# Kernel tuning notes

Hardware: AMD Instinct MI355X
Metric: run time of the kernel (lower is better)

## Reference

```python
import jax, jax.numpy as jnp
import numpy as np

NUM_EXPERTS = 8
PHM_DIM = 4


def setup_inputs() -> dict:
    key = jax.random.key(0)
    k1, k2, k3, k4 = jax.random.split(key, 4)
    bsz, seq, D, O, E, p = 4, 2048, 2048, 2048, NUM_EXPERTS, PHM_DIM
    hidden_states = jax.random.normal(k1, (bsz, seq, D), dtype=jnp.float32)
    gate_w = jax.random.normal(k2, (D, E), dtype=jnp.float32) * 0.02
    phm_rule = jax.random.normal(k3, (E, p, p, p), dtype=jnp.float32) * 0.1
    W = jax.random.normal(k4, (E, p, D // p, O // p), dtype=jnp.float32) * 0.02
    b = jnp.zeros((E, O), dtype=jnp.float32)
    return {"hidden_states": hidden_states, "gate_w": gate_w,
            "phm_rule": phm_rule, "W": W, "b": b}


def reference(hidden_states, gate_w, phm_rule, W, b):
    bsz, seq, dim = hidden_states.shape
    E = gate_w.shape[1]
    x = hidden_states.reshape(-1, dim)                      # [T, D]
    logits = x @ gate_w                                     # [T, E]
    prob = jax.nn.softmax(logits, axis=-1)                  # [T, E]
    gate = jnp.argmax(prob, axis=-1)                        # [T]
    # load-balancing loss
    num_tokens = jnp.sum(jax.nn.one_hot(gate, E, dtype=jnp.int32), axis=0)  # [E]
    f = num_tokens.astype(prob.dtype)
    f = f / jnp.sum(f)
    P = jnp.mean(prob, axis=0)
    balance_loss = E * jnp.sum(P * f)
    # PHM weight per expert: H_e = sum_p kron(phm_rule[e,p], W[e,p]) -> [E, D, O]
    Wfull = jnp.einsum('epab,epij->eaibj', phm_rule, W).reshape(E, dim, -1)
    # dense evaluation of every expert on every token, then top-1 select
    all_out = jnp.einsum('td,edo->teo', x, Wfull) + b[None, :, :]  # [T, E, O]
    tok_prob = jnp.take_along_axis(prob, gate[:, None], axis=1)    # [T, 1]
    out = jnp.take_along_axis(all_out, gate[:, None, None], axis=1)[:, 0, :] * tok_prob
    out = out.reshape(bsz, seq, -1)
    return out, balance_loss, num_tokens
```

## Files before the change

### kernel.cpp

```cpp
#include <hip/hip_runtime.h>
#include <cstdint>
#include <cstddef>

typedef _Float16 f16;
typedef f16 f16x2 __attribute__((ext_vector_type(2)));
typedef f16 f16x4 __attribute__((ext_vector_type(4)));
typedef f16 f16x8 __attribute__((ext_vector_type(8)));
typedef float f32x4 __attribute__((ext_vector_type(4)));

#define NEXP 8
#define BM 128
#define BN 128
#define BK 32
#define NSTAGE 3

__device__ __forceinline__ void async_cp16(void* lds, const void* gsrc) {
  __builtin_amdgcn_global_load_lds(
      (const __attribute__((address_space(1))) void*)gsrc,
      (__attribute__((address_space(3))) void*)lds, 16, 0, 0);
}

__global__ __launch_bounds__(256) void k_gwT(const float* __restrict__ gw,
                                             float* __restrict__ gwT, int D) {
  int i = blockIdx.x * 256 + threadIdx.x;
  int e = i / D, d = i - e * D;
  gwT[i] = gw[d * NEXP + e];
}

__global__ __launch_bounds__(256) void k_gate(
    const float* __restrict__ x, const float* __restrict__ gwT,
    f16* __restrict__ xb, int* __restrict__ gate, float* __restrict__ scale,
    int* __restrict__ cnt, float* __restrict__ probsum, int D)
{
  __shared__ float ps[NEXP];
  __shared__ int pc[NEXP];
  int tid = threadIdx.x, lane = tid & 63, w = tid >> 6;
  if (tid < NEXP) { ps[tid] = 0.f; pc[tid] = 0; }
  __syncthreads();

  int t = blockIdx.x * 4 + w;
  const float* xr = x + (size_t)t * D;
  f16* xbr = xb + (size_t)t * D;

  float acc[NEXP] = {};
  for (int d0 = lane * 4; d0 < D; d0 += 256) {
    float4 v = *(const float4*)(xr + d0);
    f16x4 h; h[0] = (f16)v.x; h[1] = (f16)v.y; h[2] = (f16)v.z; h[3] = (f16)v.w;
    *(f16x4*)(xbr + d0) = h;
#pragma unroll
    for (int e = 0; e < NEXP; e++) {
      float4 g = *(const float4*)(gwT + (size_t)e * D + d0);
      acc[e] += v.x * g.x + v.y * g.y + v.z * g.z + v.w * g.w;
    }
  }
#pragma unroll
  for (int e = 0; e < NEXP; e++) {
    float v = acc[e];
    for (int o = 32; o > 0; o >>= 1) v += __shfl_xor(v, o);
    acc[e] = v;
  }
  if (lane == 0) {
    float m = acc[0]; int g = 0;
#pragma unroll
    for (int e = 1; e < NEXP; e++) if (acc[e] > m) { m = acc[e]; g = e; }
    float pr[NEXP]; float ssum = 0.f;
#pragma unroll
    for (int e = 0; e < NEXP; e++) { pr[e] = __expf(acc[e] - m); ssum += pr[e]; }
    float inv = 1.0f / ssum;
#pragma unroll
    for (int e = 0; e < NEXP; e++) atomicAdd(&ps[e], pr[e] * inv);
    atomicAdd(&pc[g], 1);
    gate[t] = g;
    scale[t] = pr[g] * inv;
  }
  __syncthreads();
  if (tid < NEXP) {
    atomicAdd(&probsum[tid], ps[tid]);
    atomicAdd(&cnt[tid], pc[tid]);
  }
}

__global__ __launch_bounds__(256) void k_wfull(
    const float* __restrict__ Wp, const float* __restrict__ rule,
    f16* __restrict__ wt, int Dp, int Op, int D, int O)
{
  int bid = blockIdx.x;
  int it = Dp >> 5, jt = Op >> 5;
  int itile = bid % it; bid /= it;
  int jtile = bid % jt; bid /= jt;
  int e = bid;
  int i0 = itile * 32, j0 = jtile * 32;

  __shared__ float Wt[4][32][33];
  int tid = threadIdx.x;
  for (int idx = tid; idx < 4096; idx += 256) {
    int p = idx >> 10, rem = idx & 1023, ii = rem >> 5, jj = rem & 31;
    Wt[p][ii][jj] = Wp[(size_t)((e * 4 + p) * Dp + i0 + ii) * Op + j0 + jj];
  }
  __syncthreads();

  int r = tid >> 1;
  int b = r >> 5;
  int jj = r & 31;
  int h = tid & 1;

  float s[4][4];
#pragma unroll
  for (int p = 0; p < 4; p++)
#pragma unroll
    for (int a = 0; a < 4; a++)
      s[p][a] = rule[((e * 4 + p) * 4 + a) * 4 + b];

  f16x8 outv[4][2];
#pragma unroll
  for (int k = 0; k < 16; k++) {
    int i = h * 16 + k;
    float w0 = Wt[0][i][jj], w1 = Wt[1][i][jj];
    float w2 = Wt[2][i][jj], w3 = Wt[3][i][jj];
#pragma unroll
    for (int a = 0; a < 4; a++) {
      float acc = s[0][a] * w0 + s[1][a] * w1 + s[2][a] * w2 + s[3][a] * w3;
      outv[a][k >> 3][k & 7] = (f16)acc;
    }
  }

  size_t rowbase = ((size_t)e * O + (size_t)b * Op + j0 + jj) * D + i0 + h * 16;
#pragma unroll
  for (int a = 0; a < 4; a++) {
    *(f16x8*)(wt + rowbase + (size_t)a * Dp)     = outv[a][0];
    *(f16x8*)(wt + rowbase + (size_t)a * Dp + 8) = outv[a][1];
  }
}

__global__ __launch_bounds__(128) void k_plan(
    const int* __restrict__ cnt, const float* __restrict__ probsum,
    int* __restrict__ offs, int* __restrict__ ndesc,
    int2* __restrict__ desc, float* __restrict__ otail, int T)
{
  __shared__ int soffs[NEXP + 1];
  __shared__ int snd;
  __shared__ float sloss;
  __shared__ int2 sdesc[96];
  int tid = threadIdx.x;
  if (tid == 0) {
    int off = 0, nd = 0; float loss = 0.f;
    for (int e = 0; e < NEXP; e++) {
      soffs[e] = off;
      int c = cnt[e];
      loss += probsum[e] * (float)c;
      for (int m0 = 0; m0 < c; m0 += BM) { sdesc[nd] = make_int2(e, m0); nd++; }
      off += c;
    }
    soffs[NEXP] = off;
    snd = nd;
    sloss = loss;
  }
  __syncthreads();
  if (tid <= NEXP) offs[tid] = soffs[tid];
  if (tid == 9) *ndesc = snd;
  if (tid == 10) {
    float invT = 1.0f / (float)T;
    otail[0] = (float)NEXP * sloss * invT * invT;
  }
  if (tid >= 16 && tid < 16 + NEXP) otail[1 + tid - 16] = (float)cnt[tid - 16];
  for (int i = tid; i < snd; i += 128) desc[i] = sdesc[i];
}

__global__ __launch_bounds__(256) void k_scatter(
    const int* __restrict__ gate, const int* __restrict__ offs,
    int* __restrict__ cursor, int* __restrict__ perm)
{
  int t = blockIdx.x * 256 + threadIdx.x;
  int g = gate[t];
  int lane = threadIdx.x & 63;
  int pos = 0;
#pragma unroll
  for (int e = 0; e < NEXP; e++) {
    unsigned long long mask = __ballot(g == e);
    if (mask == 0ull) continue;
    int leader = __ffsll((unsigned long long)mask) - 1;
    int base = 0;
    if (lane == leader) base = atomicAdd(&cursor[e], (int)__popcll(mask));
    base = __shfl(base, leader);
    if (g == e) {
      int below = (int)__popcll(mask & ((1ull << lane) - 1ull));
      pos = offs[e] + base + below;
    }
  }
  perm[pos] = t;
}

__global__ __launch_bounds__(256) void k_gemm(
    const f16* __restrict__ xb, const f16* __restrict__ wt,
    const float* __restrict__ bias, const int* __restrict__ perm,
    const int* __restrict__ cnt, const int* __restrict__ offs,
    const int* __restrict__ ndesc, const int2* __restrict__ desc,
    const float* __restrict__ scale, float* __restrict__ out, int D, int O)
{
  if ((int)blockIdx.y >= *ndesc) return;
  int2 dsc = desc[blockIdx.y];
  int e = dsc.x, m0 = dsc.y;
  int ce = cnt[e];
  int seg = offs[e];
  int n0 = blockIdx.x * BN;

  __shared__ f16 Al[NSTAGE][BM * BK];
  __shared__ f16 Bl[NSTAGE][BN * BK];
  __shared__ int tokS[BM];
  __shared__ float scS[BM];

  int tid = threadIdx.x;
  if (tid < BM) {
    int idx = m0 + tid; if (idx > ce - 1) idx = ce - 1;
    int tok = perm[seg + idx];
    tokS[tid] = tok;
    scS[tid] = scale[tok];
  }
  __syncthreads();

  int r = tid >> 2;
  int c = tid & 3;
  int gc = c ^ ((r >> 1) & 3);
  const f16* a1 = xb + (size_t)tokS[r] * D + gc * 8;
  const f16* a2 = xb + (size_t)tokS[r + 64] * D + gc * 8;
  const f16* b1 = wt + ((size_t)e * O + n0 + r) * D + gc * 8;
  const f16* b2 = wt + ((size_t)e * O + n0 + r + 64) * D + gc * 8;

  int lane = tid & 63;
  int w = tid >> 6;
  int wm = (w & 1) * 64, wn = (w >> 1) * 64;
  int lr = lane & 15, q = lane >> 4;
  int qs = q ^ ((lr >> 1) & 3);

  f32x4 acc[4][4] = {};
  int nk = D / BK;

#define STAGE(kk, p)                                             \
  do {                                                           \
    async_cp16(&Al[(p)][tid * 8], a1 + (kk) * BK);               \
    async_cp16(&Al[(p)][2048 + tid * 8], a2 + (kk) * BK);        \
    async_cp16(&Bl[(p)][tid * 8], b1 + (kk) * BK);               \
    async_cp16(&Bl[(p)][2048 + tid * 8], b2 + (kk) * BK);        \
  } while (0)

  STAGE(0, 0);
  STAGE(1, 1);
  STAGE(2, 2);

  int p = 0;
  for (int kk = 0; kk < nk; ++kk) {
    int rem = nk - 1 - kk;
    if (rem >= 2)
      asm volatile("s_waitcnt vmcnt(8)\n\ts_barrier" ::: "memory");
    else if (rem == 1)
      asm volatile("s_waitcnt vmcnt(4)\n\ts_barrier" ::: "memory");
    else
      asm volatile("s_waitcnt vmcnt(0)\n\ts_barrier" ::: "memory");

    f16x8 af[4], bf[4];
#pragma unroll
    for (int mi = 0; mi < 4; mi++)
      af[mi] = *(const f16x8*)&Al[p][(wm + mi * 16 + lr) * BK + qs * 8];
#pragma unroll
    for (int ni = 0; ni < 4; ni++)
      bf[ni] = *(const f16x8*)&Bl[p][(wn + ni * 16 + lr) * BK + qs * 8];

    asm volatile("s_waitcnt lgkmcnt(0)\n\ts_barrier" ::: "memory");
    if (kk + NSTAGE < nk) STAGE(kk + NSTAGE, p);

#pragma unroll
    for (int mi = 0; mi < 4; mi++)
#pragma unroll
      for (int ni = 0; ni < 4; ni++)
        acc[mi][ni] = __builtin_amdgcn_mfma_f32_16x16x32_f16(
            af[mi], bf[ni], acc[mi][ni], 0, 0, 0);

    p++; if (p == NSTAGE) p = 0;
  }
#undef STAGE

  float bv[4];
#pragma unroll
  for (int ni = 0; ni < 4; ni++)
    bv[ni] = bias[(size_t)e * O + n0 + wn + ni * 16 + lr];
#pragma unroll
  for (int mi = 0; mi < 4; mi++) {
#pragma unroll
    for (int rg = 0; rg < 4; rg++) {
      int rl = wm + mi * 16 + q * 4 + rg;
      if (m0 + rl < ce) {
        float s = scS[rl];
        float* orow = out + (size_t)tokS[rl] * O + n0 + wn;
#pragma unroll
        for (int ni = 0; ni < 4; ni++)
          orow[ni * 16 + lr] = (acc[mi][ni][rg] + bv[ni]) * s;
      }
    }
  }
}

extern "C" void kernel_launch(void* const* d_in, const int* in_sizes, int n_in,
                              void* d_out, int out_size, void* d_ws, size_t ws_size,
                              hipStream_t stream)
{
  const float* x    = (const float*)d_in[0];
  const float* gw   = (const float*)d_in[1];
  const float* rule = (const float*)d_in[2];
  const float* W    = (const float*)d_in[3];
  const float* bias = (const float*)d_in[4];
  float* out = (float*)d_out;

  int D = in_sizes[1] / NEXP;
  int O = in_sizes[4] / NEXP;
  int T = in_sizes[0] / D;
  int Dp = D / 4, Op = O / 4;

  uint8_t* ws = (uint8_t*)d_ws;
  size_t off = 0;
  f16* xb = (f16*)(ws + off);  off += (size_t)T * D * 2;
  f16* wt = (f16*)(ws + off);  off += (size_t)NEXP * O * D * 2;
  int*   gate  = (int*)(ws + off);   off += (size_t)T * 4;
  float* scale = (float*)(ws + off); off += (size_t)T * 4;
  int*   perm  = (int*)(ws + off);   off += (size_t)T * 4;
  off = (off + 255) & ~(size_t)255;
  uint8_t* C = ws + off;
  int*   cnt     = (int*)(C + 0);
  float* probsum = (float*)(C + 32);
  int*   cursor  = (int*)(C + 64);
  int*   ndesc   = (int*)(C + 96);
  int*   offs    = (int*)(C + 128);
  int2*  desc    = (int2*)(C + 192);
  float* gwT     = (float*)(C + 4096);

  hipMemsetAsync(C, 0, 128, stream);

  k_gwT<<<(NEXP * D) / 256, 256, 0, stream>>>(gw, gwT, D);
  k_gate<<<T / 4, 256, 0, stream>>>(x, gwT, xb, gate, scale, cnt, probsum, D);
  k_wfull<<<NEXP * (Op / 32) * (Dp / 32), 256, 0, stream>>>(W, rule, wt, Dp, Op, D, O);
  k_plan<<<1, 128, 0, stream>>>(cnt, probsum, offs, ndesc, desc, out + (size_t)T * O, T);
  k_scatter<<<T / 256, 256, 0, stream>>>(gate, offs, cursor, perm);

  int maxdesc = T / BM + NEXP;
  k_gemm<<<dim3(O / BN, maxdesc), 256, 0, stream>>>(
      xb, wt, bias, perm, cnt, offs, ndesc, desc, scale, out, D, O);
}
```

Baseline: 344.3 us.

## Stage gate weights in LDS and process four tokens per wave in gating

The separate gate-weight transpose kernel is removed. The gating kernel now loads gate_w in 1024-column chunks into shared memory, transposing it on the fly, and each wave handles four tokens so every gate-weight load is reused across them. This cuts a kernel launch and the repeated global reads of gate weights, but it adds block barriers per chunk and more registers per thread. It assumes D is a multiple of 1024 and T is a multiple of 16.

```diff
diff --git a/kernel.cpp b/kernel.cpp
--- a/kernel.cpp
+++ b/kernel.cpp
@@ -20,58 +20,85 @@
       (__attribute__((address_space(3))) void*)lds, 16, 0, 0);
 }
 
-__global__ __launch_bounds__(256) void k_gwT(const float* __restrict__ gw,
-                                             float* __restrict__ gwT, int D) {
-  int i = blockIdx.x * 256 + threadIdx.x;
-  int e = i / D, d = i - e * D;
-  gwT[i] = gw[d * NEXP + e];
-}
-
+#define TPW 4
 __global__ __launch_bounds__(256) void k_gate(
-    const float* __restrict__ x, const float* __restrict__ gwT,
+    const float* __restrict__ x, const float* __restrict__ gw,
     f16* __restrict__ xb, int* __restrict__ gate, float* __restrict__ scale,
     int* __restrict__ cnt, float* __restrict__ probsum, int D)
 {
+  __shared__ float gws[NEXP][1028];
   __shared__ float ps[NEXP];
   __shared__ int pc[NEXP];
   int tid = threadIdx.x, lane = tid & 63, w = tid >> 6;
   if (tid < NEXP) { ps[tid] = 0.f; pc[tid] = 0; }
-  __syncthreads();
-
-  int t = blockIdx.x * 4 + w;
-  const float* xr = x + (size_t)t * D;
-  f16* xbr = xb + (size_t)t * D;
-
-  float acc[NEXP] = {};
-  for (int d0 = lane * 4; d0 < D; d0 += 256) {
-    float4 v = *(const float4*)(xr + d0);
-    f16x4 h; h[0] = (f16)v.x; h[1] = (f16)v.y; h[2] = (f16)v.z; h[3] = (f16)v.w;
-    *(f16x4*)(xbr + d0) = h;
+
+  int t0 = (blockIdx.x * 4 + w) * TPW;
+  const float* xr = x + (size_t)t0 * D;
+  f16* xbr = xb + (size_t)t0 * D;
+
+  float acc[TPW][NEXP] = {};
+  int nh = D >> 10;
+  for (int half = 0; half < nh; half++) {
+    __syncthreads();
+    const float2* gsrc = (const float2*)(gw + (size_t)half * 1024 * NEXP);
+    for (int i = tid; i < 4096; i += 256) {
+      float2 v = gsrc[i];
+      int f = i * 2;
+      int d = f >> 3, e = f & 7;
+      gws[e][d] = v.x;
+      gws[e + 1][d] = v.y;
+    }
+    __syncthreads();
+
+    int dh = half << 10;
+#pragma unroll
+    for (int it = 0; it < 4; it++) {
+      int d0 = lane * 4 + it * 256;
+      float4 xv[TPW];
+#pragma unroll
+      for (int tp = 0; tp < TPW; tp++) {
+        xv[tp] = *(const float4*)(xr + (size_t)tp * D + dh + d0);
+        f16x4 h;
+        h[0] = (f16)xv[tp].x; h[1] = (f16)xv[tp].y;
+        h[2] = (f16)xv[tp].z; h[3] = (f16)xv[tp].w;
+        *(f16x4*)(xbr + (size_t)tp * D + dh + d0) = h;
+      }
+#pragma unroll
+      for (int e = 0; e < NEXP; e++) {
+        float4 g = *(const float4*)&gws[e][d0];
+#pragma unroll
+        for (int tp = 0; tp < TPW; tp++)
+          acc[tp][e] += xv[tp].x * g.x + xv[tp].y * g.y +
+                        xv[tp].z * g.z + xv[tp].w * g.w;
+      }
+    }
+  }
+
+#pragma unroll
+  for (int tp = 0; tp < TPW; tp++)
 #pragma unroll
     for (int e = 0; e < NEXP; e++) {
-      float4 g = *(const float4*)(gwT + (size_t)e * D + d0);
-      acc[e] += v.x * g.x + v.y * g.y + v.z * g.z + v.w * g.w;
-    }
-  }
-#pragma unroll
-  for (int e = 0; e < NEXP; e++) {
-    float v = acc[e];
-    for (int o = 32; o > 0; o >>= 1) v += __shfl_xor(v, o);
-    acc[e] = v;
-  }
+      float v = acc[tp][e];
+      for (int o = 32; o > 0; o >>= 1) v += __shfl_xor(v, o);
+      acc[tp][e] = v;
+    }
+
   if (lane == 0) {
-    float m = acc[0]; int g = 0;
-#pragma unroll
-    for (int e = 1; e < NEXP; e++) if (acc[e] > m) { m = acc[e]; g = e; }
-    float pr[NEXP]; float ssum = 0.f;
-#pragma unroll
-    for (int e = 0; e < NEXP; e++) { pr[e] = __expf(acc[e] - m); ssum += pr[e]; }
-    float inv = 1.0f / ssum;
-#pragma unroll
-    for (int e = 0; e < NEXP; e++) atomicAdd(&ps[e], pr[e] * inv);
-    atomicAdd(&pc[g], 1);
-    gate[t] = g;
-    scale[t] = pr[g] * inv;
+#pragma unroll
+    for (int tp = 0; tp < TPW; tp++) {
+      float m = acc[tp][0]; int g = 0;
+#pragma unroll
+      for (int e = 1; e < NEXP; e++) if (acc[tp][e] > m) { m = acc[tp][e]; g = e; }
+      float pr[NEXP]; float ssum = 0.f;
+#pragma unroll
+      for (int e = 0; e < NEXP; e++) { pr[e] = __expf(acc[tp][e] - m); ssum += pr[e]; }
+      float inv = 1.0f / ssum;
+#pragma unroll
+      for (int e = 0; e < NEXP; e++) atomicAdd(&ps[e], pr[e] * inv);
+      atomicAdd(&pc[g], 1);
+      gate[t0 + tp] = g;
+      scale[t0 + tp] = pr[g] * inv;
+    }
   }
   __syncthreads();
   if (tid < NEXP) {
@@ -330,12 +357,10 @@
   int*   ndesc   = (int*)(C + 96);
   int*   offs    = (int*)(C + 128);
   int2*  desc    = (int2*)(C + 192);
-  float* gwT     = (float*)(C + 4096);
 
   hipMemsetAsync(C, 0, 128, stream);
 
-  k_gwT<<<(NEXP * D) / 256, 256, 0, stream>>>(gw, gwT, D);
-  k_gate<<<T / 4, 256, 0, stream>>>(x, gwT, xb, gate, scale, cnt, probsum, D);
+  k_gate<<<T / (4 * TPW), 256, 0, stream>>>(x, gw, xb, gate, scale, cnt, probsum, D);
   k_wfull<<<NEXP * (Op / 32) * (Dp / 32), 256, 0, stream>>>(W, rule, wt, Dp, Op, D, O);
   k_plan<<<1, 128, 0, stream>>>(cnt, probsum, offs, ndesc, desc, out + (size_t)T * O, T);
   k_scatter<<<T / 256, 256, 0, stream>>>(gate, offs, cursor, perm);
```

New measurement: 314.6 us. -8.6%, faster.
